# Performance work log

Hardware: AMD Instinct MI355X
Metric: run time of the kernel (lower is better)

Reference implementation:

```python
import jax, jax.numpy as jnp
import numpy as np

EMBED_DIM = 1024
NUM_HEADS = 16
HEAD_DIM = EMBED_DIM // NUM_HEADS
B, T = 2, 2048


def setup_inputs() -> dict:
    key = jax.random.key(0)
    ks = jax.random.split(key, 9)
    s = 1.0 / np.sqrt(EMBED_DIM)
    x = jax.random.normal(ks[0], (B, T, EMBED_DIM), dtype=jnp.float32)
    Wq = jax.random.uniform(ks[1], (EMBED_DIM, EMBED_DIM), jnp.float32, -s, s)
    bq = jax.random.uniform(ks[2], (EMBED_DIM,), jnp.float32, -s, s)
    Wk = jax.random.uniform(ks[3], (EMBED_DIM, EMBED_DIM), jnp.float32, -s, s)
    bk = jax.random.uniform(ks[4], (EMBED_DIM,), jnp.float32, -s, s)
    Wv = jax.random.uniform(ks[5], (EMBED_DIM, EMBED_DIM), jnp.float32, -s, s)
    bv = jax.random.uniform(ks[6], (EMBED_DIM,), jnp.float32, -s, s)
    Wo = jax.random.uniform(ks[7], (EMBED_DIM, EMBED_DIM), jnp.float32, -s, s)
    bo = jax.random.uniform(ks[8], (EMBED_DIM,), jnp.float32, -s, s)
    return {"x": x, "Wq": Wq, "bq": bq, "Wk": Wk, "bk": bk,
            "Wv": Wv, "bv": bv, "Wo": Wo, "bo": bo}


def reference(x, Wq, bq, Wk, bk, Wv, bv, Wo, bo):
    Bx, Tx, D = x.shape
    # projections (torch Linear: y = x @ W^T + b); here W stored as [in, out]
    q = (x @ Wq + bq).reshape(Bx, Tx, NUM_HEADS, HEAD_DIM).transpose(0, 2, 1, 3)
    k = (x @ Wk + bk).reshape(Bx, Tx, NUM_HEADS, HEAD_DIM).transpose(0, 2, 1, 3)
    v = (x @ Wv + bv).reshape(Bx, Tx, NUM_HEADS, HEAD_DIM).transpose(0, 2, 1, 3)
    scale = HEAD_DIM ** -0.5
    attn = jnp.einsum('bhqd,bhkd->bhqk', q, k) * scale  # [B, H, T, T]
    causal = jnp.tril(jnp.ones((Tx, Tx), dtype=bool))
    attn = jnp.where(causal[None, None], attn, -jnp.inf)
    attn = jax.nn.softmax(attn, axis=-1)
    out = jnp.einsum('bhqk,bhkd->bhqd', attn, v)  # [B, H, T, hd]
    out = out.transpose(0, 2, 1, 3).reshape(Bx, Tx, D)
    return out @ Wo + bo
```

## Files before the change

### kernel.cpp

```cpp
#include <hip/hip_runtime.h>

#define EMBED 1024
#define NHEADS 16
#define HDIM 64
#define SEQ 2048
#define BATCH 2
#define MROWS (BATCH * SEQ)

using bf16x8 = __attribute__((ext_vector_type(8))) short;
using f32x4  = __attribute__((ext_vector_type(4))) float;
using us4    = __attribute__((ext_vector_type(4))) unsigned short;
using u32x2  = __attribute__((ext_vector_type(2))) unsigned int;

__device__ __forceinline__ unsigned short f2bf(float f) {
    unsigned int u = __builtin_bit_cast(unsigned int, f);
    u = (u + 0x7fffu + ((u >> 16) & 1u)) >> 16;
    return (unsigned short)u;
}

__device__ __forceinline__ unsigned int cvt_pk_bf16(float a, float b) {
    unsigned int d;
    asm("v_cvt_pk_bf16_f32 %0, %1, %2" : "=v"(d) : "v"(a), "v"(b));
    return d;
}

__device__ __forceinline__ void async16(const unsigned short* g, unsigned short* l) {
    __builtin_amdgcn_global_load_lds(
        (const __attribute__((address_space(1))) void*)g,
        (__attribute__((address_space(3))) void*)l, 16, 0, 0);
}

__global__ __launch_bounds__(256)
void cvt_x(const float* __restrict__ in, unsigned short* __restrict__ out)
{
    int i = blockIdx.x * 256 + threadIdx.x;
    float4 v = ((const float4*)in)[i];
    us4 o;
    o[0] = f2bf(v.x); o[1] = f2bf(v.y); o[2] = f2bf(v.z); o[3] = f2bf(v.w);
    ((us4*)out)[i] = o;
}

__global__ __launch_bounds__(256)
void cvt_w(const float* __restrict__ W0, const float* __restrict__ W1,
           const float* __restrict__ W2, const float* __restrict__ W3,
           unsigned short* __restrict__ T0, unsigned short* __restrict__ T1,
           unsigned short* __restrict__ T2, unsigned short* __restrict__ T3)
{
    const float* W = blockIdx.z == 0 ? W0 : blockIdx.z == 1 ? W1 :
                     blockIdx.z == 2 ? W2 : W3;
    unsigned short* T = blockIdx.z == 0 ? T0 : blockIdx.z == 1 ? T1 :
                        blockIdx.z == 2 ? T2 : T3;
    __shared__ unsigned short tile[64][72];
    const int tid = threadIdx.x;
    const int k0 = blockIdx.y << 6, n0 = blockIdx.x << 6;
    const int lr = tid >> 4, lc = (tid & 15) << 2;
#pragma unroll
    for (int it = 0; it < 4; ++it) {
        int kr = lr + it * 16;
        float4 v = *(const float4*)(W + (size_t)(k0 + kr) * EMBED + n0 + lc);
        tile[lc + 0][kr] = f2bf(v.x);
        tile[lc + 1][kr] = f2bf(v.y);
        tile[lc + 2][kr] = f2bf(v.z);
        tile[lc + 3][kr] = f2bf(v.w);
    }
    __syncthreads();
#pragma unroll
    for (int it = 0; it < 4; ++it) {
        int nr = lr + it * 16;
        us4 o = *(const us4*)(&tile[nr][lc]);
        *(us4*)(T + (size_t)(n0 + nr) * EMBED + k0 + lc) = o;
    }
}

__device__ __forceinline__ void mfma_gemm_core(
    const unsigned short* __restrict__ A, const unsigned short* __restrict__ Bt,
    int bm, int n0, unsigned short* As, unsigned short* Bs,
    int wv, int lane, f32x4 acc[4][4])
{
    const int m16 = lane & 15, quad = lane >> 4;
    const int mb = (wv >> 1) << 6;
    const int nb = (wv & 1) << 6;

    const unsigned short* ga = A  + (size_t)(bm + wv * 32 + (lane >> 3)) * EMBED + ((lane & 7) << 3);
    const unsigned short* gb = Bt + (size_t)(n0 + wv * 32 + (lane >> 3)) * EMBED + ((lane & 7) << 3);
    unsigned short* la = As + wv * 32 * 64;
    unsigned short* lb = Bs + wv * 32 * 64;

    for (int k0 = 0; k0 < EMBED; k0 += 64) {
        __syncthreads();
#pragma unroll
        for (int j = 0; j < 4; ++j) {
            async16(ga + j * 8 * EMBED, la + j * 8 * 64);
            async16(gb + j * 8 * EMBED, lb + j * 8 * 64);
        }
        ga += 64; gb += 64;
        __syncthreads();
#pragma unroll
        for (int ks = 0; ks < 2; ++ks) {
            const int ko = ks * 32 + (quad << 3);
            bf16x8 af[4], bfv[4];
#pragma unroll
            for (int i = 0; i < 4; ++i) {
                af[i]  = *(const bf16x8*)(As + (mb + i * 16 + m16) * 64 + ko);
                bfv[i] = *(const bf16x8*)(Bs + (nb + i * 16 + m16) * 64 + ko);
            }
#pragma unroll
            for (int i = 0; i < 4; ++i)
#pragma unroll
                for (int j = 0; j < 4; ++j)
                    acc[i][j] = __builtin_amdgcn_mfma_f32_16x16x32_bf16(
                        af[i], bfv[j], acc[i][j], 0, 0, 0);
        }
    }
}

__device__ __forceinline__ void mfma_gemm_core64(
    const unsigned short* __restrict__ A, const unsigned short* __restrict__ Bt,
    int bm, int n0, unsigned short* As, unsigned short* Bs,
    int wv, int lane, f32x4 acc[4][2])
{
    const int m16 = lane & 15, quad = lane >> 4;
    const int mb = (wv >> 1) << 6;
    const int nb = (wv & 1) << 5;

    const unsigned short* ga = A  + (size_t)(bm + wv * 32 + (lane >> 3)) * EMBED + ((lane & 7) << 3);
    const unsigned short* gb = Bt + (size_t)(n0 + wv * 16 + (lane >> 3)) * EMBED + ((lane & 7) << 3);
    unsigned short* la = As + wv * 32 * 64;
    unsigned short* lb = Bs + wv * 16 * 64;

    for (int k0 = 0; k0 < EMBED; k0 += 64) {
        __syncthreads();
#pragma unroll
        for (int j = 0; j < 4; ++j)
            async16(ga + j * 8 * EMBED, la + j * 8 * 64);
#pragma unroll
        for (int j = 0; j < 2; ++j)
            async16(gb + j * 8 * EMBED, lb + j * 8 * 64);
        ga += 64; gb += 64;
        __syncthreads();
#pragma unroll
        for (int ks = 0; ks < 2; ++ks) {
            const int ko = ks * 32 + (quad << 3);
            bf16x8 af[4], bfv[2];
#pragma unroll
            for (int i = 0; i < 4; ++i)
                af[i] = *(const bf16x8*)(As + (mb + i * 16 + m16) * 64 + ko);
#pragma unroll
            for (int j = 0; j < 2; ++j)
                bfv[j] = *(const bf16x8*)(Bs + (nb + j * 16 + m16) * 64 + ko);
#pragma unroll
            for (int i = 0; i < 4; ++i)
#pragma unroll
                for (int j = 0; j < 2; ++j)
                    acc[i][j] = __builtin_amdgcn_mfma_f32_16x16x32_bf16(
                        af[i], bfv[j], acc[i][j], 0, 0, 0);
        }
    }
}

__global__ __launch_bounds__(256)
void qkv_gemm(const unsigned short* __restrict__ xb,
              const unsigned short* __restrict__ Wtq,
              const unsigned short* __restrict__ Wtk,
              const unsigned short* __restrict__ Wtv,
              const float* __restrict__ bq, const float* __restrict__ bk,
              const float* __restrict__ bv,
              unsigned short* __restrict__ Qo, unsigned short* __restrict__ Ko,
              unsigned short* __restrict__ Vto)
{
    __shared__ __align__(16) unsigned short As[128 * 64];
    __shared__ __align__(16) unsigned short Bs[128 * 64];
    const int tid = threadIdx.x, wv = tid >> 6, lane = tid & 63;
    const int m16 = lane & 15, quad = lane >> 4;
    const int which = blockIdx.x >> 3;
    const int n0 = (blockIdx.x & 7) << 7;
    const int bm = blockIdx.y << 7;
    const unsigned short* Bt = which == 0 ? Wtq : which == 1 ? Wtk : Wtv;
    const float* bias = which == 0 ? bq : which == 1 ? bk : bv;

    f32x4 acc[4][4];
#pragma unroll
    for (int i = 0; i < 4; ++i)
#pragma unroll
        for (int j = 0; j < 4; ++j) acc[i][j] = (f32x4){0.f, 0.f, 0.f, 0.f};

    mfma_gemm_core(xb, Bt, bm, n0, As, Bs, wv, lane, acc);

    const int mb = (wv >> 1) << 6, nb = (wv & 1) << 6;
    const float qscale = 0.125f * 1.4426950408889634f;
#pragma unroll
    for (int i = 0; i < 4; ++i) {
        const int m0 = bm + mb + i * 16 + quad * 4;
        const int b = m0 >> 11, t0 = m0 & (SEQ - 1);
#pragma unroll
        for (int j = 0; j < 4; ++j) {
            const int n = n0 + nb + j * 16 + m16;
            const int h = n >> 6, d = n & 63;
            const float bval = bias[n];
            if (which == 2) {
                us4 v;
#pragma unroll
                for (int r = 0; r < 4; ++r) v[r] = f2bf(acc[i][j][r] + bval);
                *(us4*)(Vto + ((((size_t)(b * NHEADS + h)) << 6) + d) * SEQ + t0) = v;
            } else {
                const float sc = which == 0 ? qscale : 1.f;
                unsigned short* dst = (which == 0 ? Qo : Ko) +
                    ((((size_t)(b * NHEADS + h)) << 11) + t0) * 64 + d;
#pragma unroll
                for (int r = 0; r < 4; ++r)
                    dst[(size_t)r * 64] = f2bf((acc[i][j][r] + bval) * sc);
            }
        }
    }
}

__global__ __launch_bounds__(256)
void out_gemm(const unsigned short* __restrict__ aob,
              const unsigned short* __restrict__ Wto,
              const float* __restrict__ bo, float* __restrict__ out)
{
    __shared__ __align__(16) unsigned short As[128 * 64];
    __shared__ __align__(16) unsigned short Bs[64 * 64];
    const int tid = threadIdx.x, wv = tid >> 6, lane = tid & 63;
    const int m16 = lane & 15, quad = lane >> 4;
    const int n0 = blockIdx.x << 6;
    const int bm = blockIdx.y << 7;

    f32x4 acc[4][2];
#pragma unroll
    for (int i = 0; i < 4; ++i)
#pragma unroll
        for (int j = 0; j < 2; ++j) acc[i][j] = (f32x4){0.f, 0.f, 0.f, 0.f};

    mfma_gemm_core64(aob, Wto, bm, n0, As, Bs, wv, lane, acc);

    const int mb = (wv >> 1) << 6, nb = (wv & 1) << 5;
#pragma unroll
    for (int i = 0; i < 4; ++i) {
        const int m0 = bm + mb + i * 16 + quad * 4;
#pragma unroll
        for (int j = 0; j < 2; ++j) {
            const int n = n0 + nb + j * 16 + m16;
            const float bval = bo[n];
#pragma unroll
            for (int r = 0; r < 4; ++r)
                out[(size_t)(m0 + r) * EMBED + n] = acc[i][j][r] + bval;
        }
    }
}

__global__ __launch_bounds__(256)
void attn_mfma(const unsigned short* __restrict__ Qb,
               const unsigned short* __restrict__ Kb,
               const unsigned short* __restrict__ Vtb,
               unsigned short* __restrict__ Oout)
{
    __shared__ __align__(16) unsigned short Ks[2][64 * 64];
    __shared__ __align__(16) unsigned short Vt[2][64 * 64];
    __shared__ __align__(16) unsigned short Ps[4][16 * 64];

    const int tid  = threadIdx.x;
    const int wv   = tid >> 6;
    const int lane = tid & 63;
    const int m16  = lane & 15;
    const int quad = lane >> 4;
    const int bh   = blockIdx.x;
    const int b    = bh >> 4, h = bh & 15;

    const int yr = blockIdx.y & 7, yk = blockIdx.y >> 3;
    const int qt = yk == 0 ? yr : yk == 1 ? 15 - yr : yk == 2 ? 16 + yr : 31 - yr;
    const int q0 = qt << 6;

    const int srow = tid >> 2;
    const int cc   = tid & 3;
    const int swr  = srow & 7;
    const int sx   = m16 & 7;

    bf16x8 rk0, rk1, rv0, rv1;
    auto load_tile = [&](int k0) {
        const int scol = cc << 4;
        const unsigned short* sk = Kb + (((size_t)bh << 11) + k0 + srow) * 64 + scol;
        rk0 = *(const bf16x8*)sk;
        rk1 = *(const bf16x8*)(sk + 8);
        const unsigned short* sv = Vtb + (((size_t)bh << 6) + srow) * SEQ + k0 + scol;
        rv0 = *(const bf16x8*)sv;
        rv1 = *(const bf16x8*)(sv + 8);
    };

    const size_t qoff =
        (((size_t)bh << 11) + q0 + (wv << 4) + m16) * 64 + (quad << 3);
    bf16x8 qa0 = *(const bf16x8*)(Qb + qoff);
    bf16x8 qa1 = *(const bf16x8*)(Qb + qoff + 32);

    f32x4 o[4];
#pragma unroll
    for (int dt = 0; dt < 4; ++dt) o[dt] = (f32x4){0.f, 0.f, 0.f, 0.f};
    float m_ = -1e30f, l_ = 0.f;

    load_tile(0);

    for (int kt = 0; kt <= qt; ++kt) {
        unsigned short* Kp = Ks[kt & 1];
        unsigned short* Vp = Vt[kt & 1];
        {
            unsigned short* kd = Kp + srow * 64;
            unsigned short* vd = Vp + srow * 64;
            *(bf16x8*)(kd + (((2 * cc) ^ swr) << 3))     = rk0;
            *(bf16x8*)(kd + (((2 * cc + 1) ^ swr) << 3)) = rk1;
            *(bf16x8*)(vd + (((2 * cc) ^ swr) << 3))     = rv0;
            *(bf16x8*)(vd + (((2 * cc + 1) ^ swr) << 3)) = rv1;
        }
        __syncthreads();
        if (kt < qt) load_tile((kt + 1) << 6);

        const bool diag = (kt == qt);

        f32x4 s[4];
#pragma unroll
        for (int g = 0; g < 4; ++g) {
            if (diag && g > wv) {
                s[g] = (f32x4){-1e30f, -1e30f, -1e30f, -1e30f};
                continue;
            }
            const unsigned short* kr = Kp + (g * 16 + m16) * 64;
            bf16x8 kb0 = *(const bf16x8*)(kr + ((quad ^ sx) << 3));
            bf16x8 kb1 = *(const bf16x8*)(kr + (((quad + 4) ^ sx) << 3));
            s[g] = (f32x4){0.f, 0.f, 0.f, 0.f};
            s[g] = __builtin_amdgcn_mfma_f32_16x16x32_bf16(kb0, qa0, s[g], 0, 0, 0);
            s[g] = __builtin_amdgcn_mfma_f32_16x16x32_bf16(kb1, qa1, s[g], 0, 0, 0);
        }
        if (diag) {
#pragma unroll
            for (int r = 0; r < 4; ++r)
                if (quad * 4 + r > m16) s[wv][r] = -1e30f;
        }

        float mx = fmaxf(fmaxf(s[0][0], s[0][1]), fmaxf(s[0][2], s[0][3]));
#pragma unroll
        for (int g = 1; g < 4; ++g)
            mx = fmaxf(mx, fmaxf(fmaxf(s[g][0], s[g][1]), fmaxf(s[g][2], s[g][3])));
        mx = fmaxf(mx, __shfl_xor(mx, 16));
        mx = fmaxf(mx, __shfl_xor(mx, 32));

        if (mx > m_ + 8.f) {
            const float alpha = exp2f(m_ - mx);
            m_ = mx;
            l_ *= alpha;
#pragma unroll
            for (int dt = 0; dt < 4; ++dt) o[dt] *= alpha;
        }

        float sum = 0.f;
        unsigned int pw0[4], pw1[4];
#pragma unroll
        for (int g = 0; g < 4; ++g) {
            float p0 = exp2f(s[g][0] - m_);
            float p1 = exp2f(s[g][1] - m_);
            float p2 = exp2f(s[g][2] - m_);
            float p3 = exp2f(s[g][3] - m_);
            sum += (p0 + p1) + (p2 + p3);
            pw0[g] = cvt_pk_bf16(p0, p1);
            pw1[g] = cvt_pk_bf16(p2, p3);
        }
        sum += __shfl_xor(sum, 16);
        sum += __shfl_xor(sum, 32);
        l_ += sum;

        {
            unsigned short* pd = Ps[wv] + m16 * 64 + ((quad & 1) << 2);
#pragma unroll
            for (int g = 0; g < 4; ++g) {
                u32x2 w; w.x = pw0[g]; w.y = pw1[g];
                *(u32x2*)(pd + (((2 * g + (quad >> 1)) ^ sx) << 3)) = w;
            }
        }

        const unsigned short* pr = Ps[wv] + m16 * 64;
        bf16x8 pa0 = *(const bf16x8*)(pr + ((quad ^ sx) << 3));
        bf16x8 pa1 = *(const bf16x8*)(pr + (((quad + 4) ^ sx) << 3));
        const bool skip_hi = diag && (wv < 2);
#pragma unroll
        for (int dt = 0; dt < 4; ++dt) {
            const unsigned short* vr = Vp + (dt * 16 + m16) * 64;
            bf16x8 vb0 = *(const bf16x8*)(vr + ((quad ^ sx) << 3));
            o[dt] = __builtin_amdgcn_mfma_f32_16x16x32_bf16(vb0, pa0, o[dt], 0, 0, 0);
            if (!skip_hi) {
                bf16x8 vb1 = *(const bf16x8*)(vr + (((quad + 4) ^ sx) << 3));
                o[dt] = __builtin_amdgcn_mfma_f32_16x16x32_bf16(vb1, pa1, o[dt], 0, 0, 0);
            }
        }
    }

    const float inv = 1.f / l_;
    const int t = q0 + (wv << 4) + m16;
    unsigned short* dst =
        Oout + ((size_t)((b << 11) + t) << 10) + (h << 6) + (quad << 2);
#pragma unroll
    for (int dt = 0; dt < 4; ++dt) {
        u32x2 w;
        w.x = cvt_pk_bf16(o[dt][0] * inv, o[dt][1] * inv);
        w.y = cvt_pk_bf16(o[dt][2] * inv, o[dt][3] * inv);
        *(u32x2*)(dst + dt * 16) = w;
    }
}

extern "C" void kernel_launch(void* const* d_in, const int* in_sizes, int n_in,
                              void* d_out, int out_size, void* d_ws, size_t ws_size,
                              hipStream_t stream) {
    const float* x  = (const float*)d_in[0];
    const float* Wq = (const float*)d_in[1];
    const float* bq = (const float*)d_in[2];
    const float* Wk = (const float*)d_in[3];
    const float* bk = (const float*)d_in[4];
    const float* Wv = (const float*)d_in[5];
    const float* bv = (const float*)d_in[6];
    const float* Wo = (const float*)d_in[7];
    const float* bo = (const float*)d_in[8];
    float* out = (float*)d_out;

    const size_t HSZ = (size_t)MROWS * EMBED;
    const size_t WSZ = (size_t)EMBED * EMBED;
    unsigned short* qb  = (unsigned short*)d_ws;
    unsigned short* kb  = qb + HSZ;
    unsigned short* vtb = kb + HSZ;
    unsigned short* aob = vtb + HSZ;
    unsigned short* xb  = aob + HSZ;
    unsigned short* wtq = xb + HSZ;
    unsigned short* wtk = wtq + WSZ;
    unsigned short* wtv = wtk + WSZ;
    unsigned short* wto = wtv + WSZ;

    cvt_x<<<MROWS * EMBED / 1024, 256, 0, stream>>>(x, xb);
    cvt_w<<<dim3(16, 16, 4), 256, 0, stream>>>(Wq, Wk, Wv, Wo, wtq, wtk, wtv, wto);

    qkv_gemm<<<dim3(24, 32), 256, 0, stream>>>(xb, wtq, wtk, wtv, bq, bk, bv,
                                               qb, kb, vtb);

    attn_mfma<<<dim3(32, 32), 256, 0, stream>>>(qb, kb, vtb, aob);

    out_gemm<<<dim3(16, 32), 256, 0, stream>>>(aob, wto, bo, out);
}
```

Baseline: 213.8 us.

## Double-buffer GEMM LDS tiles with async prefetch and XOR-swizzled layout

Both projection GEMM cores now use two LDS buffers, so the async global-to-LDS copy of the next K tile is issued before the MFMAs on the current one, with explicit vmcnt waits and barriers. The global column offsets and LDS read offsets are XOR-swizzled by row so that the 16-byte fragment reads avoid LDS bank conflicts. LDS use per block doubles, which may lower occupancy. The attention kernel, which likely accounts for most of the time, is unchanged.

New measurement: 202.8 us. 5.1% less time.

```diff
diff --git a/kernel.cpp b/kernel.cpp
--- a/kernel.cpp
+++ b/kernel.cpp
@@ -80,29 +80,51 @@
     const int m16 = lane & 15, quad = lane >> 4;
     const int mb = (wv >> 1) << 6;
     const int nb = (wv & 1) << 6;
-
-    const unsigned short* ga = A  + (size_t)(bm + wv * 32 + (lane >> 3)) * EMBED + ((lane & 7) << 3);
-    const unsigned short* gb = Bt + (size_t)(n0 + wv * 32 + (lane >> 3)) * EMBED + ((lane & 7) << 3);
-    unsigned short* la = As + wv * 32 * 64;
-    unsigned short* lb = Bs + wv * 32 * 64;
-
-    for (int k0 = 0; k0 < EMBED; k0 += 64) {
-        __syncthreads();
-#pragma unroll
-        for (int j = 0; j < 4; ++j) {
-            async16(ga + j * 8 * EMBED, la + j * 8 * 64);
-            async16(gb + j * 8 * EMBED, lb + j * 8 * 64);
-        }
-        ga += 64; gb += 64;
-        __syncthreads();
+    const int rsw = m16 & 7;
+
+    const int gcol = ((lane & 7) ^ ((lane >> 3) & 7)) << 3;
+    const unsigned short* ga = A  + (size_t)(bm + wv * 32 + (lane >> 3)) * EMBED + gcol;
+    const unsigned short* gb = Bt + (size_t)(n0 + wv * 32 + (lane >> 3)) * EMBED + gcol;
+
+    int offA[4], offB[4];
+#pragma unroll
+    for (int i = 0; i < 4; ++i) {
+        offA[i] = (mb + i * 16 + m16) * 64;
+        offB[i] = (nb + i * 16 + m16) * 64;
+    }
+
+    const int NK = EMBED / 64;
+#define STAGE(t) do {                                                        \
+        unsigned short* la = As + ((t) & 1) * (128 * 64) + wv * 32 * 64;     \
+        unsigned short* lb = Bs + ((t) & 1) * (128 * 64) + wv * 32 * 64;     \
+        const unsigned short* gat = ga + (t) * 64;                           \
+        const unsigned short* gbt = gb + (t) * 64;                           \
+        _Pragma("unroll")                                                    \
+        for (int j = 0; j < 4; ++j) {                                        \
+            async16(gat + j * 8 * EMBED, la + j * 8 * 64);                   \
+            async16(gbt + j * 8 * EMBED, lb + j * 8 * 64);                   \
+        }                                                                    \
+    } while (0)
+
+    STAGE(0);
+    for (int t = 0; t < NK; ++t) {
+        if (t + 1 < NK) {
+            STAGE(t + 1);
+            asm volatile("s_waitcnt vmcnt(8)" ::: "memory");
+        } else {
+            asm volatile("s_waitcnt vmcnt(0)" ::: "memory");
+        }
+        asm volatile("s_barrier" ::: "memory");
+        const unsigned short* Ab = As + (t & 1) * (128 * 64);
+        const unsigned short* Bb = Bs + (t & 1) * (128 * 64);
 #pragma unroll
         for (int ks = 0; ks < 2; ++ks) {
-            const int ko = ks * 32 + (quad << 3);
+            const int sl = (((ks << 2) + quad) ^ rsw) << 3;
             bf16x8 af[4], bfv[4];
 #pragma unroll
             for (int i = 0; i < 4; ++i) {
-                af[i]  = *(const bf16x8*)(As + (mb + i * 16 + m16) * 64 + ko);
-                bfv[i] = *(const bf16x8*)(Bs + (nb + i * 16 + m16) * 64 + ko);
+                af[i]  = *(const bf16x8*)(Ab + offA[i] + sl);
+                bfv[i] = *(const bf16x8*)(Bb + offB[i] + sl);
             }
 #pragma unroll
             for (int i = 0; i < 4; ++i)
@@ -111,7 +133,9 @@
                     acc[i][j] = __builtin_amdgcn_mfma_f32_16x16x32_bf16(
                         af[i], bfv[j], acc[i][j], 0, 0, 0);
         }
-    }
+        asm volatile("s_barrier" ::: "memory");
+    }
+#undef STAGE
 }
 
 __device__ __forceinline__ void mfma_gemm_core64(
@@ -122,32 +146,53 @@
     const int m16 = lane & 15, quad = lane >> 4;
     const int mb = (wv >> 1) << 6;
     const int nb = (wv & 1) << 5;
-
-    const unsigned short* ga = A  + (size_t)(bm + wv * 32 + (lane >> 3)) * EMBED + ((lane & 7) << 3);
-    const unsigned short* gb = Bt + (size_t)(n0 + wv * 16 + (lane >> 3)) * EMBED + ((lane & 7) << 3);
-    unsigned short* la = As + wv * 32 * 64;
-    unsigned short* lb = Bs + wv * 16 * 64;
-
-    for (int k0 = 0; k0 < EMBED; k0 += 64) {
-        __syncthreads();
-#pragma unroll
-        for (int j = 0; j < 4; ++j)
-            async16(ga + j * 8 * EMBED, la + j * 8 * 64);
-#pragma unroll
-        for (int j = 0; j < 2; ++j)
-            async16(gb + j * 8 * EMBED, lb + j * 8 * 64);
-        ga += 64; gb += 64;
-        __syncthreads();
+    const int rsw = m16 & 7;
+
+    const int gcol = ((lane & 7) ^ ((lane >> 3) & 7)) << 3;
+    const unsigned short* ga = A  + (size_t)(bm + wv * 32 + (lane >> 3)) * EMBED + gcol;
+    const unsigned short* gb = Bt + (size_t)(n0 + wv * 16 + (lane >> 3)) * EMBED + gcol;
+
+    int offA[4], offB[2];
+#pragma unroll
+    for (int i = 0; i < 4; ++i) offA[i] = (mb + i * 16 + m16) * 64;
+#pragma unroll
+    for (int j = 0; j < 2; ++j) offB[j] = (nb + j * 16 + m16) * 64;
+
+    const int NK = EMBED / 64;
+#define STAGE64(t) do {                                                      \
+        unsigned short* la = As + ((t) & 1) * (128 * 64) + wv * 32 * 64;     \
+        unsigned short* lb = Bs + ((t) & 1) * (64 * 64) + wv * 16 * 64;      \
+        const unsigned short* gat = ga + (t) * 64;                           \
+        const unsigned short* gbt = gb + (t) * 64;                           \
+        _Pragma("unroll")                                                    \
+        for (int j = 0; j < 4; ++j)                                          \
+            async16(gat + j * 8 * EMBED, la + j * 8 * 64);                   \
+        _Pragma("unroll")                                                    \
+        for (int j = 0; j < 2; ++j)                                          \
+            async16(gbt + j * 8 * EMBED, lb + j * 8 * 64);                   \
+    } while (0)
+
+    STAGE64(0);
+    for (int t = 0; t < NK; ++t) {
+        if (t + 1 < NK) {
+            STAGE64(t + 1);
+            asm volatile("s_waitcnt vmcnt(6)" ::: "memory");
+        } else {
+            asm volatile("s_waitcnt vmcnt(0)" ::: "memory");
+        }
+        asm volatile("s_barrier" ::: "memory");
+        const unsigned short* Ab = As + (t & 1) * (128 * 64);
+        const unsigned short* Bb = Bs + (t & 1) * (64 * 64);
 #pragma unroll
         for (int ks = 0; ks < 2; ++ks) {
-            const int ko = ks * 32 + (quad << 3);
+            const int sl = (((ks << 2) + quad) ^ rsw) << 3;
             bf16x8 af[4], bfv[2];
 #pragma unroll
             for (int i = 0; i < 4; ++i)
-                af[i] = *(const bf16x8*)(As + (mb + i * 16 + m16) * 64 + ko);
+                af[i] = *(const bf16x8*)(Ab + offA[i] + sl);
 #pragma unroll
             for (int j = 0; j < 2; ++j)
-                bfv[j] = *(const bf16x8*)(Bs + (nb + j * 16 + m16) * 64 + ko);
+                bfv[j] = *(const bf16x8*)(Bb + offB[j] + sl);
 #pragma unroll
             for (int i = 0; i < 4; ++i)
 #pragma unroll
@@ -155,7 +200,9 @@
                     acc[i][j] = __builtin_amdgcn_mfma_f32_16x16x32_bf16(
                         af[i], bfv[j], acc[i][j], 0, 0, 0);
         }
-    }
+        asm volatile("s_barrier" ::: "memory");
+    }
+#undef STAGE64
 }
 
 __global__ __launch_bounds__(256)
@@ -168,8 +215,8 @@
               unsigned short* __restrict__ Qo, unsigned short* __restrict__ Ko,
               unsigned short* __restrict__ Vto)
 {
-    __shared__ __align__(16) unsigned short As[128 * 64];
-    __shared__ __align__(16) unsigned short Bs[128 * 64];
+    __shared__ __align__(16) unsigned short As[2 * 128 * 64];
+    __shared__ __align__(16) unsigned short Bs[2 * 128 * 64];
     const int tid = threadIdx.x, wv = tid >> 6, lane = tid & 63;
     const int m16 = lane & 15, quad = lane >> 4;
     const int which = blockIdx.x >> 3;
@@ -219,8 +266,8 @@
               const unsigned short* __restrict__ Wto,
               const float* __restrict__ bo, float* __restrict__ out)
 {
-    __shared__ __align__(16) unsigned short As[128 * 64];
-    __shared__ __align__(16) unsigned short Bs[64 * 64];
+    __shared__ __align__(16) unsigned short As[2 * 128 * 64];
+    __shared__ __align__(16) unsigned short Bs[2 * 64 * 64];
     const int tid = threadIdx.x, wv = tid >> 6, lane = tid & 63;
     const int m16 = lane & 15, quad = lane >> 4;
     const int n0 = blockIdx.x << 6;
```
